# Optimization experiments

Hardware: AMD Instinct MI355X
Metric: run time of the kernel (lower is better)

The kernel has to match this reference:

```python
import jax, jax.numpy as jnp
import numpy as np

B, C, H, W = 64, 64, 128, 128


def setup_inputs() -> dict:
    key = jax.random.key(0)
    x = jax.random.normal(key, (B, C, H, W), dtype=jnp.float32)
    return {"x": x, "topk": 256}


def reference(x, topk):
    b = x.shape[0]
    xf = x.reshape(b, -1)                      # [B, N]
    _, idx = jax.lax.top_k(jnp.abs(xf), topk)  # [B, K] indices of largest |x|
    vals = jnp.take_along_axis(xf, idx, axis=-1)  # gather original (signed) values
    rows = jnp.arange(b)[:, None]
    out = jnp.zeros_like(xf).at[rows, idx].set(vals)  # scatter into zeros
    return out.reshape(x.shape)
```

## Files before the change

### kernel.cpp

```cpp
#include <hip/hip_runtime.h>
#include <stdint.h>


#define NBINS 4096
#define ROWS  64
#define HBLK  8
#define FBLK  32
#define MAXCAP 16384u
#define LDS_SEL 2048

__global__ void hist_kernel(const float* __restrict__ x, unsigned* __restrict__ parts,
                            int n_per_row) {
    __shared__ unsigned lh[NBINS];
    for (int i = threadIdx.x; i < NBINS; i += blockDim.x) lh[i] = 0;
    __syncthreads();

    int row = blockIdx.x / HBLK;
    int sub = blockIdx.x % HBLK;
    int chunk = n_per_row / HBLK;
    const float4* xv = (const float4*)(x + (size_t)row * n_per_row + (size_t)sub * chunk);
    int nvec = chunk / 4;
    for (int i = threadIdx.x; i < nvec; i += blockDim.x) {
        float4 v = xv[i];
        atomicAdd(&lh[(__float_as_uint(v.x) & 0x7fffffffu) >> 19], 1u);
        atomicAdd(&lh[(__float_as_uint(v.y) & 0x7fffffffu) >> 19], 1u);
        atomicAdd(&lh[(__float_as_uint(v.z) & 0x7fffffffu) >> 19], 1u);
        atomicAdd(&lh[(__float_as_uint(v.w) & 0x7fffffffu) >> 19], 1u);
    }
    __syncthreads();

    unsigned* gp = parts + (size_t)blockIdx.x * NBINS;
    for (int i = threadIdx.x; i < NBINS; i += blockDim.x) gp[i] = lh[i];
}

__global__ void cutoff_kernel(const unsigned* __restrict__ parts,
                              const int* __restrict__ topk,
                              unsigned* __restrict__ row_b, unsigned* __restrict__ row_r) {
    __shared__ unsigned h[NBINS];
    __shared__ unsigned csum[256];
    int row = blockIdx.x;
    const unsigned* base = parts + (size_t)row * HBLK * NBINS;
    for (int i = threadIdx.x; i < NBINS; i += blockDim.x) {
        unsigned s = 0;
        #pragma unroll
        for (int p = 0; p < HBLK; ++p) s += base[(size_t)p * NBINS + i];
        h[i] = s;
    }
    __syncthreads();

    const int CHUNK = NBINS / 256;
    unsigned cs = 0;
    int cbase = threadIdx.x * CHUNK;
    #pragma unroll
    for (int j = 0; j < CHUNK; ++j) cs += h[cbase + j];
    csum[threadIdx.x] = cs;
    __syncthreads();

    if (threadIdx.x == 0) {
        unsigned K = (unsigned)(*topk);
        unsigned acc = 0;
        int chunk = 255;
        for (; chunk > 0; --chunk) {
            if (acc + csum[chunk] >= K) break;
            acc += csum[chunk];
        }
        unsigned bstar = (unsigned)(chunk * CHUNK);
        for (int b = chunk * CHUNK + CHUNK - 1; b >= chunk * CHUNK; --b) {
            unsigned c = h[b];
            if (acc + c >= K) { bstar = (unsigned)b; break; }
            acc += c;
        }
        row_b[row] = bstar;
        row_r[row] = K - acc;
    }
}

__global__ void filter_kernel(const float* __restrict__ x, float* __restrict__ out,
                              const unsigned* __restrict__ row_b,
                              unsigned* __restrict__ cand_count,
                              uint2* __restrict__ cand, unsigned cap,
                              int n_per_row) {
    int row = blockIdx.x / FBLK;
    int sub = blockIdx.x % FBLK;
    int chunk = n_per_row / FBLK;
    size_t base_e = (size_t)row * n_per_row + (size_t)sub * chunk;
    const float4* xv = (const float4*)(x + base_e);
    float4* ov = (float4*)(out + base_e);
    unsigned idx_base = (unsigned)(sub * chunk);
    unsigned bstar = row_b[row];
    int nvec = chunk / 4;
    for (int i = threadIdx.x; i < nvec; i += blockDim.x) {
        float4 v = xv[i];
        float in[4] = {v.x, v.y, v.z, v.w};
        float o[4];
        #pragma unroll
        for (int c = 0; c < 4; ++c) {
            unsigned bits = __float_as_uint(in[c]);
            unsigned bin  = (bits & 0x7fffffffu) >> 19;
            o[c] = (bin > bstar) ? in[c] : 0.0f;
            if (bin == bstar) {
                unsigned pos = atomicAdd(&cand_count[row], 1u);
                if (pos < cap) cand[(size_t)row * cap + pos] =
                    make_uint2(bits, idx_base + (unsigned)i * 4u + (unsigned)c);
            }
        }
        ov[i] = make_float4(o[0], o[1], o[2], o[3]);
    }
}

__global__ void select_kernel(const unsigned* __restrict__ cand_count,
                              const uint2* __restrict__ cand, unsigned cap,
                              const unsigned* __restrict__ row_r,
                              float* __restrict__ out, int n_per_row) {
    __shared__ uint2 lc[LDS_SEL];
    int row = blockIdx.x;
    unsigned M = cand_count[row];
    if (M > cap) M = cap;
    unsigned r = row_r[row];
    const uint2* c = cand + (size_t)row * cap;
    if (M <= LDS_SEL) {
        for (unsigned i = threadIdx.x; i < M; i += blockDim.x) lc[i] = c[i];
        __syncthreads();
        for (unsigned i = threadIdx.x; i < M; i += blockDim.x) {
            uint2 ci = lc[i];
            unsigned ai = ci.x & 0x7fffffffu;
            unsigned rank = 0;
            for (unsigned j = 0; j < M; ++j) {
                uint2 cj = lc[j];
                unsigned aj = cj.x & 0x7fffffffu;
                rank += (unsigned)((aj > ai) || (aj == ai && cj.y < ci.y));
            }
            if (rank < r)
                out[(size_t)row * n_per_row + ci.y] = __uint_as_float(ci.x);
        }
    } else {
        for (unsigned i = threadIdx.x; i < M; i += blockDim.x) {
            uint2 ci = c[i];
            unsigned ai = ci.x & 0x7fffffffu;
            unsigned rank = 0;
            for (unsigned j = 0; j < M; ++j) {
                uint2 cj = c[j];
                unsigned aj = cj.x & 0x7fffffffu;
                rank += (unsigned)((aj > ai) || (aj == ai && cj.y < ci.y));
            }
            if (rank < r)
                out[(size_t)row * n_per_row + ci.y] = __uint_as_float(ci.x);
        }
    }
}

extern "C" void kernel_launch(void* const* d_in, const int* in_sizes, int n_in,
                              void* d_out, int out_size, void* d_ws, size_t ws_size,
                              hipStream_t stream) {
    const float* x   = (const float*)d_in[0];
    const int* topk  = (const int*)d_in[1];
    float* out       = (float*)d_out;

    const int rows = ROWS;
    const int n_per_row = out_size / rows;

    uint8_t* ws = (uint8_t*)d_ws;
    size_t off = 0;
    unsigned* parts = (unsigned*)(ws + off);
    off += (size_t)rows * HBLK * NBINS * sizeof(unsigned);
    unsigned* cand_count = (unsigned*)(ws + off); off += 256;
    unsigned* row_b      = (unsigned*)(ws + off); off += 256;
    unsigned* row_r      = (unsigned*)(ws + off); off += 256;
    off = (off + 255) & ~(size_t)255;
    size_t avail = (ws_size > off) ? (ws_size - off) : 0;
    unsigned cap = (unsigned)(avail / ((size_t)rows * sizeof(uint2)));
    if (cap > MAXCAP) cap = MAXCAP;
    if (cap == 0) cap = 1;
    uint2* cand = (uint2*)(ws + off);

    hipMemsetAsync((void*)cand_count, 0, 256, stream);

    hist_kernel<<<rows * HBLK, 512, 0, stream>>>(x, parts, n_per_row);
    cutoff_kernel<<<rows, 256, 0, stream>>>(parts, topk, row_b, row_r);
    filter_kernel<<<rows * FBLK, 256, 0, stream>>>(x, out, row_b, cand_count, cand,
                                                   cap, n_per_row);
    select_kernel<<<rows, 256, 0, stream>>>(cand_count, cand, cap, row_r, out, n_per_row);
}
```

Baseline: 531.6 us.

## Collect large-magnitude candidates during histogram pass, replace full filter read with memset

The histogram kernel now counts only the upper half of exponent bins and, at the same time, stashes elements above a fixed magnitude threshold into a per-row candidate list. This removes the second full read of the input that the old filter kernel needed. The output is zeroed with a memset, and a small compact kernel scatters the values above the cutoff bin and gathers the tie-bin candidates for the select step. A per-row fallback kernel redoes the full histogram and filter when the fixed threshold or the buffer capacities turn out to be too small. That fallback is much slower, since it runs one block per row.

```diff
diff --git a/kernel.cpp b/kernel.cpp
--- a/kernel.cpp
+++ b/kernel.cpp
@@ -2,53 +2,92 @@
 #include <stdint.h>
 
 
-#define NBINS 4096
+#define NBINS   4096
+#define TBINS   2048
+#define TB_BASE 2048u
+#define G_COLLECT 2052u
 #define ROWS  64
 #define HBLK  8
-#define FBLK  32
-#define MAXCAP 16384u
+#define CBLK  4
+#define LC_CAP 4096
 #define LDS_SEL 2048
 
-__global__ void hist_kernel(const float* __restrict__ x, unsigned* __restrict__ parts,
-                            int n_per_row) {
-    __shared__ unsigned lh[NBINS];
-    for (int i = threadIdx.x; i < NBINS; i += blockDim.x) lh[i] = 0;
+__global__ __launch_bounds__(512) void hist_collect_kernel(
+    const float* __restrict__ x, unsigned* __restrict__ parts,
+    unsigned* __restrict__ cand_count, uint2* __restrict__ cand, unsigned cap1,
+    unsigned* __restrict__ row_over, int n_per_row)
+{
+    __shared__ unsigned lh[TBINS];
+    __shared__ uint2 lc[LC_CAP];
+    __shared__ unsigned lcnt;
+    __shared__ unsigned gbase;
+    for (int i = threadIdx.x; i < TBINS; i += blockDim.x) lh[i] = 0;
+    if (threadIdx.x == 0) lcnt = 0;
     __syncthreads();
 
     int row = blockIdx.x / HBLK;
     int sub = blockIdx.x % HBLK;
     int chunk = n_per_row / HBLK;
     const float4* xv = (const float4*)(x + (size_t)row * n_per_row + (size_t)sub * chunk);
+    unsigned idx_base = (unsigned)(sub * chunk);
     int nvec = chunk / 4;
     for (int i = threadIdx.x; i < nvec; i += blockDim.x) {
         float4 v = xv[i];
-        atomicAdd(&lh[(__float_as_uint(v.x) & 0x7fffffffu) >> 19], 1u);
-        atomicAdd(&lh[(__float_as_uint(v.y) & 0x7fffffffu) >> 19], 1u);
-        atomicAdd(&lh[(__float_as_uint(v.z) & 0x7fffffffu) >> 19], 1u);
-        atomicAdd(&lh[(__float_as_uint(v.w) & 0x7fffffffu) >> 19], 1u);
-    }
-    __syncthreads();
-
-    unsigned* gp = parts + (size_t)blockIdx.x * NBINS;
-    for (int i = threadIdx.x; i < NBINS; i += blockDim.x) gp[i] = lh[i];
-}
-
-__global__ void cutoff_kernel(const unsigned* __restrict__ parts,
-                              const int* __restrict__ topk,
-                              unsigned* __restrict__ row_b, unsigned* __restrict__ row_r) {
-    __shared__ unsigned h[NBINS];
+        unsigned bb[4] = {__float_as_uint(v.x), __float_as_uint(v.y),
+                          __float_as_uint(v.z), __float_as_uint(v.w)};
+        #pragma unroll
+        for (int c = 0; c < 4; ++c) {
+            unsigned bin = (bb[c] & 0x7fffffffu) >> 19;
+            if (bin >= TB_BASE) {
+                atomicAdd(&lh[bin - TB_BASE], 1u);
+                if (bin >= G_COLLECT) {
+                    unsigned pos = atomicAdd(&lcnt, 1u);
+                    if (pos < (unsigned)LC_CAP)
+                        lc[pos] = make_uint2(bb[c],
+                                             idx_base + (unsigned)i * 4u + (unsigned)c);
+                }
+            }
+        }
+    }
+    __syncthreads();
+
+    unsigned* gp = parts + (size_t)blockIdx.x * TBINS;
+    for (int i = threadIdx.x; i < TBINS; i += blockDim.x) gp[i] = lh[i];
+
+    unsigned n = lcnt;
+    if (threadIdx.x == 0) {
+        unsigned nn = (n > (unsigned)LC_CAP) ? (unsigned)LC_CAP : n;
+        gbase = atomicAdd(&cand_count[row], nn);
+        if (n > (unsigned)LC_CAP || gbase + nn > cap1) atomicOr(&row_over[row], 1u);
+    }
+    if (n > (unsigned)LC_CAP) n = (unsigned)LC_CAP;
+    __syncthreads();
+    unsigned base = gbase;
+    for (unsigned i = threadIdx.x; i < n; i += blockDim.x) {
+        unsigned p = base + i;
+        if (p < cap1) cand[(size_t)row * cap1 + p] = lc[i];
+    }
+}
+
+__global__ __launch_bounds__(256) void cutoff_kernel(
+    const unsigned* __restrict__ parts, const int* __restrict__ topk,
+    const unsigned* __restrict__ row_over,
+    unsigned* __restrict__ row_b, unsigned* __restrict__ row_r,
+    unsigned* __restrict__ row_ok)
+{
+    __shared__ unsigned h[TBINS];
     __shared__ unsigned csum[256];
     int row = blockIdx.x;
-    const unsigned* base = parts + (size_t)row * HBLK * NBINS;
-    for (int i = threadIdx.x; i < NBINS; i += blockDim.x) {
+    const unsigned* base = parts + (size_t)row * HBLK * TBINS;
+    for (int i = threadIdx.x; i < TBINS; i += blockDim.x) {
         unsigned s = 0;
         #pragma unroll
-        for (int p = 0; p < HBLK; ++p) s += base[(size_t)p * NBINS + i];
+        for (int p = 0; p < HBLK; ++p) s += base[(size_t)p * TBINS + i];
         h[i] = s;
     }
     __syncthreads();
 
-    const int CHUNK = NBINS / 256;
+    const int CHUNK = TBINS / 256;
     unsigned cs = 0;
     int cbase = threadIdx.x * CHUNK;
     #pragma unroll
@@ -59,65 +98,119 @@
     if (threadIdx.x == 0) {
         unsigned K = (unsigned)(*topk);
         unsigned acc = 0;
-        int chunk = 255;
-        for (; chunk > 0; --chunk) {
-            if (acc + csum[chunk] >= K) break;
-            acc += csum[chunk];
-        }
-        unsigned bstar = (unsigned)(chunk * CHUNK);
-        for (int b = chunk * CHUNK + CHUNK - 1; b >= chunk * CHUNK; --b) {
+        int found = 0, ch;
+        for (ch = 255; ch >= 0; --ch) {
+            if (acc + csum[ch] >= K) { found = 1; break; }
+            acc += csum[ch];
+        }
+        unsigned okf = 0;
+        if (found) {
+            int b = ch * CHUNK + CHUNK - 1;
+            for (; b > ch * CHUNK; --b) {
+                unsigned c = h[b];
+                if (acc + c >= K) break;
+                acc += c;
+            }
+            unsigned bstar = (unsigned)b + TB_BASE;
+            row_b[row] = bstar;
+            row_r[row] = K - acc;
+            okf = (bstar >= G_COLLECT && row_over[row] == 0) ? 1u : 0u;
+        }
+        row_ok[row] = okf;
+    }
+}
+
+__global__ __launch_bounds__(256) void compact_kernel(
+    const unsigned* __restrict__ cand_count, const uint2* __restrict__ cand,
+    unsigned cap1, const unsigned* __restrict__ row_ok,
+    const unsigned* __restrict__ row_b,
+    unsigned* __restrict__ cand2_count, uint2* __restrict__ cand2, unsigned cap2,
+    float* __restrict__ out, int n_per_row)
+{
+    int row = blockIdx.x / CBLK;
+    if (!row_ok[row]) return;
+    unsigned bstar = row_b[row];
+    unsigned M = cand_count[row]; if (M > cap1) M = cap1;
+    const uint2* c = cand + (size_t)row * cap1;
+    int sub = blockIdx.x % CBLK;
+    for (unsigned i = (unsigned)sub * blockDim.x + threadIdx.x; i < M;
+         i += blockDim.x * CBLK) {
+        uint2 e = c[i];
+        unsigned bin = (e.x & 0x7fffffffu) >> 19;
+        if (bin > bstar) {
+            out[(size_t)row * n_per_row + e.y] = __uint_as_float(e.x);
+        } else if (bin == bstar) {
+            unsigned pos = atomicAdd(&cand2_count[row], 1u);
+            if (pos < cap2) cand2[(size_t)row * cap2 + pos] = e;
+        }
+    }
+}
+
+__global__ __launch_bounds__(256) void fallback_kernel(
+    const float* __restrict__ x, const int* __restrict__ topk,
+    const unsigned* __restrict__ row_ok, unsigned* __restrict__ row_r,
+    unsigned* __restrict__ cand2_count, uint2* __restrict__ cand2, unsigned cap2,
+    float* __restrict__ out, int n_per_row)
+{
+    __shared__ unsigned h[NBINS];
+    __shared__ unsigned csum[256];
+    __shared__ unsigned sb;
+    int row = blockIdx.x;
+    if (row_ok[row]) return;
+
+    for (int i = threadIdx.x; i < NBINS; i += blockDim.x) h[i] = 0;
+    __syncthreads();
+    const float* xr = x + (size_t)row * n_per_row;
+    for (int i = threadIdx.x; i < n_per_row; i += blockDim.x)
+        atomicAdd(&h[(__float_as_uint(xr[i]) & 0x7fffffffu) >> 19], 1u);
+    __syncthreads();
+
+    const int CHUNK = NBINS / 256;
+    unsigned cs = 0;
+    for (int j = 0; j < CHUNK; ++j) cs += h[threadIdx.x * CHUNK + j];
+    csum[threadIdx.x] = cs;
+    __syncthreads();
+
+    if (threadIdx.x == 0) {
+        unsigned K = (unsigned)(*topk);
+        unsigned acc = 0;
+        int ch = 255;
+        for (; ch > 0; --ch) { if (acc + csum[ch] >= K) break; acc += csum[ch]; }
+        int b = ch * CHUNK + CHUNK - 1;
+        for (; b > ch * CHUNK; --b) {
             unsigned c = h[b];
-            if (acc + c >= K) { bstar = (unsigned)b; break; }
+            if (acc + c >= K) break;
             acc += c;
         }
-        row_b[row] = bstar;
+        sb = (unsigned)b;
         row_r[row] = K - acc;
     }
-}
-
-__global__ void filter_kernel(const float* __restrict__ x, float* __restrict__ out,
-                              const unsigned* __restrict__ row_b,
-                              unsigned* __restrict__ cand_count,
-                              uint2* __restrict__ cand, unsigned cap,
-                              int n_per_row) {
-    int row = blockIdx.x / FBLK;
-    int sub = blockIdx.x % FBLK;
-    int chunk = n_per_row / FBLK;
-    size_t base_e = (size_t)row * n_per_row + (size_t)sub * chunk;
-    const float4* xv = (const float4*)(x + base_e);
-    float4* ov = (float4*)(out + base_e);
-    unsigned idx_base = (unsigned)(sub * chunk);
-    unsigned bstar = row_b[row];
-    int nvec = chunk / 4;
-    for (int i = threadIdx.x; i < nvec; i += blockDim.x) {
-        float4 v = xv[i];
-        float in[4] = {v.x, v.y, v.z, v.w};
-        float o[4];
-        #pragma unroll
-        for (int c = 0; c < 4; ++c) {
-            unsigned bits = __float_as_uint(in[c]);
-            unsigned bin  = (bits & 0x7fffffffu) >> 19;
-            o[c] = (bin > bstar) ? in[c] : 0.0f;
-            if (bin == bstar) {
-                unsigned pos = atomicAdd(&cand_count[row], 1u);
-                if (pos < cap) cand[(size_t)row * cap + pos] =
-                    make_uint2(bits, idx_base + (unsigned)i * 4u + (unsigned)c);
-            }
-        }
-        ov[i] = make_float4(o[0], o[1], o[2], o[3]);
-    }
-}
-
-__global__ void select_kernel(const unsigned* __restrict__ cand_count,
-                              const uint2* __restrict__ cand, unsigned cap,
-                              const unsigned* __restrict__ row_r,
-                              float* __restrict__ out, int n_per_row) {
+    __syncthreads();
+
+    unsigned bstar = sb;
+    for (int i = threadIdx.x; i < n_per_row; i += blockDim.x) {
+        unsigned bits = __float_as_uint(xr[i]);
+        unsigned bin = (bits & 0x7fffffffu) >> 19;
+        if (bin > bstar) {
+            out[(size_t)row * n_per_row + i] = __uint_as_float(bits);
+        } else if (bin == bstar) {
+            unsigned pos = atomicAdd(&cand2_count[row], 1u);
+            if (pos < cap2) cand2[(size_t)row * cap2 + pos] = make_uint2(bits, (unsigned)i);
+        }
+    }
+}
+
+__global__ __launch_bounds__(256) void select_kernel(
+    const unsigned* __restrict__ cand2_count, const uint2* __restrict__ cand2,
+    unsigned cap2, const unsigned* __restrict__ row_r,
+    float* __restrict__ out, int n_per_row)
+{
     __shared__ uint2 lc[LDS_SEL];
     int row = blockIdx.x;
-    unsigned M = cand_count[row];
-    if (M > cap) M = cap;
+    unsigned M = cand2_count[row];
+    if (M > cap2) M = cap2;
     unsigned r = row_r[row];
-    const uint2* c = cand + (size_t)row * cap;
+    const uint2* c = cand2 + (size_t)row * cap2;
     if (M <= LDS_SEL) {
         for (unsigned i = threadIdx.x; i < M; i += blockDim.x) lc[i] = c[i];
         __syncthreads();
@@ -152,9 +245,9 @@
 extern "C" void kernel_launch(void* const* d_in, const int* in_sizes, int n_in,
                               void* d_out, int out_size, void* d_ws, size_t ws_size,
                               hipStream_t stream) {
-    const float* x   = (const float*)d_in[0];
-    const int* topk  = (const int*)d_in[1];
-    float* out       = (float*)d_out;
+    const float* x  = (const float*)d_in[0];
+    const int* topk = (const int*)d_in[1];
+    float* out      = (float*)d_out;
 
     const int rows = ROWS;
     const int n_per_row = out_size / rows;
@@ -162,22 +255,36 @@
     uint8_t* ws = (uint8_t*)d_ws;
     size_t off = 0;
     unsigned* parts = (unsigned*)(ws + off);
-    off += (size_t)rows * HBLK * NBINS * sizeof(unsigned);
-    unsigned* cand_count = (unsigned*)(ws + off); off += 256;
-    unsigned* row_b      = (unsigned*)(ws + off); off += 256;
-    unsigned* row_r      = (unsigned*)(ws + off); off += 256;
+    off += (size_t)rows * HBLK * TBINS * sizeof(unsigned);
+    unsigned* cand_count  = (unsigned*)(ws + off); off += 256;
+    unsigned* cand2_count = (unsigned*)(ws + off); off += 256;
+    unsigned* row_over    = (unsigned*)(ws + off); off += 256;
+    unsigned* row_b       = (unsigned*)(ws + off); off += 256;
+    unsigned* row_r       = (unsigned*)(ws + off); off += 256;
+    unsigned* row_ok      = (unsigned*)(ws + off); off += 256;
     off = (off + 255) & ~(size_t)255;
+
     size_t avail = (ws_size > off) ? (ws_size - off) : 0;
-    unsigned cap = (unsigned)(avail / ((size_t)rows * sizeof(uint2)));
-    if (cap > MAXCAP) cap = MAXCAP;
-    if (cap == 0) cap = 1;
-    uint2* cand = (uint2*)(ws + off);
-
-    hipMemsetAsync((void*)cand_count, 0, 256, stream);
-
-    hist_kernel<<<rows * HBLK, 512, 0, stream>>>(x, parts, n_per_row);
-    cutoff_kernel<<<rows, 256, 0, stream>>>(parts, topk, row_b, row_r);
-    filter_kernel<<<rows * FBLK, 256, 0, stream>>>(x, out, row_b, cand_count, cand,
-                                                   cap, n_per_row);
-    select_kernel<<<rows, 256, 0, stream>>>(cand_count, cand, cap, row_r, out, n_per_row);
-}
+    size_t entries = avail / ((size_t)rows * sizeof(uint2));
+    unsigned cap1 = 32768u, cap2 = 16384u;
+    if (entries < (size_t)(cap1 + cap2)) {
+        cap2 = (unsigned)(entries / 3); if (cap2 == 0) cap2 = 1;
+        cap1 = (unsigned)(entries - cap2); if (cap1 == 0) cap1 = 1;
+    }
+    uint2* cand  = (uint2*)(ws + off); off += (size_t)rows * cap1 * sizeof(uint2);
+    uint2* cand2 = (uint2*)(ws + off);
+
+    hipMemsetAsync((void*)cand_count, 0, 768, stream);
+    hipMemsetAsync((void*)out, 0, (size_t)out_size * sizeof(float), stream);
+
+    hist_collect_kernel<<<rows * HBLK, 512, 0, stream>>>(x, parts, cand_count, cand,
+                                                         cap1, row_over, n_per_row);
+    cutoff_kernel<<<rows, 256, 0, stream>>>(parts, topk, row_over, row_b, row_r, row_ok);
+    compact_kernel<<<rows * CBLK, 256, 0, stream>>>(cand_count, cand, cap1, row_ok,
+                                                    row_b, cand2_count, cand2, cap2,
+                                                    out, n_per_row);
+    fallback_kernel<<<rows, 256, 0, stream>>>(x, topk, row_ok, row_r,
+                                              cand2_count, cand2, cap2, out, n_per_row);
+    select_kernel<<<rows, 256, 0, stream>>>(cand2_count, cand2, cap2, row_r,
+                                            out, n_per_row);
+}
```

Result: faster. 513.0 us (-3.5%).
